# Performance work log

Measured on AMD Instinct MI355X. Metric: run time of the kernel, lower is better.

The kernel has to match this reference:

```python
import jax, jax.numpy as jnp
import numpy as np

B, DIM, H, W = 8, 96, 256, 256
NH, WS, SS = 3, 8, 4
HD = DIM // NH
SCALE = HD ** -0.5
N = WS * WS  # tokens per window


def _rel_pos_log(ws):
    # [N, N, 2] signed log relative coordinates (matches get_relative_positions)
    coords = np.stack(np.meshgrid(np.arange(ws), np.arange(ws), indexing='ij'))
    cf = coords.reshape(2, -1)
    rel = (cf[:, :, None] - cf[:, None, :]).transpose(1, 2, 0).astype(np.float32)
    return np.sign(rel) * np.log1p(np.abs(rel))


def _attn_mask(Hh, Ww, ws, ss):
    # Swin shifted-window mask: [nW, N, N] with 0 / -100
    img = np.zeros((Hh, Ww))
    cnt = 0
    sl = (slice(0, -ws), slice(-ws, -ss), slice(-ss, None))
    for h in sl:
        for w in sl:
            img[h, w] = cnt
            cnt += 1
    mw = img.reshape(Hh // ws, ws, Ww // ws, ws).transpose(0, 2, 1, 3).reshape(-1, ws * ws)
    am = mw[:, None, :] - mw[:, :, None]
    return np.where(am != 0, -100.0, 0.0).astype(np.float32)


REL_POS = jnp.asarray(_rel_pos_log(WS))        # [N, N, 2]
ATTN_MASK = jnp.asarray(_attn_mask(H, W, WS, SS))  # [nW, N, N]


def setup_inputs() -> dict:
    key = jax.random.key(0)
    ks = jax.random.split(key, 8)
    s = 0.02
    return {
        'x': jax.random.normal(ks[0], (B, DIM, H, W), jnp.float32),
        'V_w': jax.random.normal(ks[1], (DIM, DIM), jnp.float32) * s,
        'V_b': jnp.zeros((DIM,), jnp.float32),
        'QK_w': jax.random.normal(ks[2], (2 * DIM, DIM), jnp.float32) * s,
        'QK_b': jnp.zeros((2 * DIM,), jnp.float32),
        'proj_w': jax.random.normal(ks[3], (DIM, DIM), jnp.float32) * s,
        'proj_b': jnp.zeros((DIM,), jnp.float32),
        'dw_w': jax.random.normal(ks[4], (DIM, 5, 5), jnp.float32) * s,
        'dw_b': jnp.zeros((DIM,), jnp.float32),
        'meta_w1': jax.random.normal(ks[5], (256, 2), jnp.float32) * 0.1,
        'meta_b1': jnp.zeros((256,), jnp.float32),
        'meta_w2': jax.random.normal(ks[6], (NH, 256), jnp.float32) * 0.1,
        'meta_b2': jnp.zeros((NH,), jnp.float32),
    }


def reference(x, V_w, V_b, QK_w, QK_b, proj_w, proj_b, dw_w, dw_b,
              meta_w1, meta_b1, meta_w2, meta_b2):
    # 1x1 convs as channel matmuls
    V = jnp.einsum('bchw,oc->bohw', x, V_w) + V_b[None, :, None, None]
    QK = jnp.einsum('bchw,oc->bohw', x, QK_w) + QK_b[None, :, None, None]
    qkv = jnp.concatenate([QK, V], axis=1).transpose(0, 2, 3, 1)  # [B,H,W,3C]
    # cyclic shift
    qkv = jnp.roll(qkv, (-SS, -SS), axis=(1, 2))
    # window partition -> [B*nW, N, 3C]
    xw = qkv.reshape(B, H // WS, WS, W // WS, WS, 3 * DIM)
    xw = xw.transpose(0, 1, 3, 2, 4, 5).reshape(-1, N, 3 * DIM)
    qkv3 = xw.reshape(-1, N, 3, NH, HD).transpose(2, 0, 3, 1, 4)  # [3, B_, nh, N, hd]
    q, k, v = qkv3[0] * SCALE, qkv3[1], qkv3[2]
    attn = jnp.einsum('whnd,whmd->whnm', q, k)  # [B_, nh, N, N]
    # MLP relative-position bias
    bias = jax.nn.relu(REL_POS @ meta_w1.T + meta_b1) @ meta_w2.T + meta_b2  # [N,N,nh]
    attn = attn + bias.transpose(2, 0, 1)[None]
    nW = ATTN_MASK.shape[0]
    attn = attn.reshape(B, nW, NH, N, N) + ATTN_MASK[None, :, None]
    attn = jax.nn.softmax(attn, axis=-1).reshape(-1, NH, N, N)
    xo = jnp.einsum('whnm,whmd->wnhd', attn, v).reshape(-1, N, DIM)
    # window reverse -> [B,H,W,C]
    xr = xo.reshape(B, H // WS, W // WS, WS, WS, DIM)
    xr = xr.transpose(0, 1, 3, 2, 4, 5).reshape(B, H, W, DIM)
    xr = jnp.roll(xr, (SS, SS), axis=(1, 2)).transpose(0, 3, 1, 2)  # [B,C,H,W]
    # depthwise 5x5 conv with reflect padding on V
    Vp = jnp.pad(V, ((0, 0), (0, 0), (2, 2), (2, 2)), mode='reflect')
    conv_out = jax.lax.conv_general_dilated(
        Vp, dw_w.reshape(DIM, 1, 5, 5), (1, 1), 'VALID',
        feature_group_count=DIM,
        dimension_numbers=('NCHW', 'OIHW', 'NCHW')) + dw_b[None, :, None, None]
    out = jnp.einsum('bchw,oc->bohw', conv_out + xr, proj_w) + proj_b[None, :, None, None]
    return out
```

## Files before the change

kernel.cpp:

```cpp
#include <hip/hip_runtime.h>
#include <hip/hip_bf16.h>

#define HW 65536
#define SCALE_Q 0.17677669529663687f

typedef __bf16 bf16x8 __attribute__((ext_vector_type(8)));
typedef float f32x4 __attribute__((ext_vector_type(4)));

__global__ void bias_kernel(const float* __restrict__ w1, const float* __restrict__ b1,
                            const float* __restrict__ w2, const float* __restrict__ b2,
                            float* __restrict__ biasF) {
    int gid = blockIdx.x * blockDim.x + threadIdx.x;
    if (gid >= 12288) return;
    int lane = gid & 63, r = (gid >> 6) & 3, ni = (gid >> 8) & 3, mi = (gid >> 10) & 3, h = gid >> 12;
    int i = mi * 16 + ((lane >> 4) << 2) + r;
    int j = ni * 16 + (lane & 15);
    float di = (float)((i >> 3) - (j >> 3));
    float dj = (float)((i & 7) - (j & 7));
    float r0 = (di > 0.f ? 1.f : (di < 0.f ? -1.f : 0.f)) * log1pf(fabsf(di));
    float r1 = (dj > 0.f ? 1.f : (dj < 0.f ? -1.f : 0.f)) * log1pf(fabsf(dj));
    float acc = 0.f;
    for (int t = 0; t < 256; ++t) {
        float u = fmaf(w1[2 * t], r0, fmaf(w1[2 * t + 1], r1, b1[t]));
        u = fmaxf(u, 0.f);
        acc = fmaf(w2[h * 256 + t], u, acc);
    }
    biasF[gid] = acc + b2[h];
}

__global__ void wtrans_kernel(const float* __restrict__ QK_w, const float* __restrict__ V_w,
                              const float* __restrict__ proj_w,
                              __bf16* __restrict__ Whi, __bf16* __restrict__ Wlo,
                              __bf16* __restrict__ WpHi, __bf16* __restrict__ WpLo) {
    int idx = blockIdx.x * blockDim.x + threadIdx.x;
    if (idx < 288 * 96) {
        int oo = idx / 96, c = idx - oo * 96;
        int h = oo / 96, rem = oo - h * 96, grp = rem >> 5, d = rem & 31;
        float w = (grp == 0) ? QK_w[(h * 32 + d) * 96 + c]
                : (grp == 1) ? QK_w[(96 + h * 32 + d) * 96 + c]
                             : V_w[(h * 32 + d) * 96 + c];
        __bf16 hi = (__bf16)w;
        Whi[idx] = hi;
        Wlo[idx] = (__bf16)(w - (float)hi);
    } else if (idx < 288 * 96 + 96 * 96) {
        int rdx = idx - 288 * 96;
        float w = proj_w[rdx];
        __bf16 hi = (__bf16)w;
        WpHi[rdx] = hi;
        WpLo[rdx] = (__bf16)(w - (float)hi);
    }
}

template <bool XRB>
__global__ __launch_bounds__(256, 3) void fused_qkv_attn(
    const float* __restrict__ x,
    const __bf16* __restrict__ Whi, const __bf16* __restrict__ Wlo,
    const float* __restrict__ QK_b, const float* __restrict__ V_b,
    const float* __restrict__ biasF,
    unsigned short* __restrict__ Vout, void* __restrict__ xrv) {
    __shared__ __align__(16) char lds[53376];
    int tid = threadIdx.x;
    int w4 = tid >> 6;
    int lane = tid & 63;
    int l16 = lane & 15;
    int g8 = (lane >> 4) << 3;
    int g4 = (lane >> 4) << 2;
    int bx0 = blockIdx.x;
    int bxs = (bx0 & 7) * 256 + (bx0 >> 3);
    int b = bxs >> 8;
    int wh = (bxs >> 3) & 31;
    int ww0 = (bxs & 7) << 2;
    int wh8 = wh << 3;
    int wb8 = ww0 << 3;
    int ww = ww0 + w4;
    int ti = lane >> 3, tj = lane & 7;
    int ph = (wh8 + ti + 4) & 255;
    int pw = ((ww << 3) + tj + 4) & 255;
    int pos   = ph * 256 + pw;
    int pos_s = (wh8 + ti) * 256 + (ww << 3) + tj;

    __bf16* Xh = (__bf16*)lds;
    const float* xb = x + (size_t)b * 96 * HW;
    for (int idx = tid; idx < 24576; idx += 256) {
        int c = idx >> 8, r = (idx >> 5) & 7, col = idx & 31;
        int pph = (wh8 + r + 4) & 255;
        int ppw = (wb8 + col + 4) & 255;
        Xh[(col >> 3) * 6672 + (r * 8 + (col & 7)) * 104 + c] =
            (__bf16)xb[(size_t)c * HW + pph * 256 + ppw];
    }
    __syncthreads();

    bf16x8 Ah[4][3];
    const __bf16* Xw = Xh + w4 * 6672;
#pragma unroll
    for (int mi = 0; mi < 4; ++mi)
#pragma unroll
        for (int ks = 0; ks < 3; ++ks)
            Ah[mi][ks] = *(const bf16x8*)(Xw + (mi * 16 + l16) * 104 + ks * 32 + g8);
    __syncthreads();

    char* hb = lds + w4 * 9984;
    __bf16* slab = (__bf16*)hb;
    __bf16* Vt   = (__bf16*)(hb + 5120);
    float*  Xr   = (float*)hb;

    bool bhh = (wh == 31), bww = (ww == 31);
    int rc[4];
#pragma unroll
    for (int ni = 0; ni < 4; ++ni) {
        int t = ni * 16 + l16;
        rc[ni] = (bhh ? (((t >> 3) < 4) ? 1 : 2) : 0) * 3 + (bww ? (((t & 7) < 4) ? 1 : 2) : 0);
    }

#pragma unroll 1
    for (int h = 0; h < 3; ++h) {
        bf16x8 Qf[4], Kf[4];
        {
            f32x4 acc[4][2];
#pragma unroll
            for (int mi = 0; mi < 4; ++mi)
#pragma unroll
                for (int ni = 0; ni < 2; ++ni) acc[mi][ni] = (f32x4){0.f, 0.f, 0.f, 0.f};
            __builtin_amdgcn_s_setprio(1);
#pragma unroll
            for (int ks = 0; ks < 3; ++ks)
#pragma unroll
                for (int ni = 0; ni < 2; ++ni) {
                    bf16x8 Bh = *(const bf16x8*)(Whi + (h * 96 + ni * 16 + l16) * 96 + ks * 32 + g8);
#pragma unroll
                    for (int mi = 0; mi < 4; ++mi)
                        acc[mi][ni] = __builtin_amdgcn_mfma_f32_16x16x32_bf16(Ah[mi][ks], Bh, acc[mi][ni], 0, 0, 0);
                }
            __builtin_amdgcn_s_setprio(0);
#pragma unroll
            for (int ni = 0; ni < 2; ++ni) {
                float bias = QK_b[h * 32 + ni * 16 + l16];
#pragma unroll
                for (int mi = 0; mi < 4; ++mi)
#pragma unroll
                    for (int r = 0; r < 4; ++r)
                        slab[(mi * 16 + g4 + r) * 40 + ni * 16 + l16] = (__bf16)((acc[mi][ni][r] + bias) * SCALE_Q);
            }
#pragma unroll
            for (int mi = 0; mi < 4; ++mi) Qf[mi] = *(const bf16x8*)(slab + (mi * 16 + l16) * 40 + g8);
        }
        {
            f32x4 acc[4][2];
#pragma unroll
            for (int mi = 0; mi < 4; ++mi)
#pragma unroll
                for (int ni = 0; ni < 2; ++ni) acc[mi][ni] = (f32x4){0.f, 0.f, 0.f, 0.f};
            __builtin_amdgcn_s_setprio(1);
#pragma unroll
            for (int ks = 0; ks < 3; ++ks)
#pragma unroll
                for (int ni = 0; ni < 2; ++ni) {
                    bf16x8 Bh = *(const bf16x8*)(Whi + (h * 96 + 32 + ni * 16 + l16) * 96 + ks * 32 + g8);
#pragma unroll
                    for (int mi = 0; mi < 4; ++mi)
                        acc[mi][ni] = __builtin_amdgcn_mfma_f32_16x16x32_bf16(Ah[mi][ks], Bh, acc[mi][ni], 0, 0, 0);
                }
            __builtin_amdgcn_s_setprio(0);
#pragma unroll
            for (int ni = 0; ni < 2; ++ni) {
                float bias = QK_b[96 + h * 32 + ni * 16 + l16];
#pragma unroll
                for (int mi = 0; mi < 4; ++mi)
#pragma unroll
                    for (int r = 0; r < 4; ++r)
                        slab[(mi * 16 + g4 + r) * 40 + ni * 16 + l16] = (__bf16)(acc[mi][ni][r] + bias);
            }
#pragma unroll
            for (int mi = 0; mi < 4; ++mi) Kf[mi] = *(const bf16x8*)(slab + (mi * 16 + l16) * 40 + g8);
        }
        {
            f32x4 acc[4][2];
#pragma unroll
            for (int mi = 0; mi < 4; ++mi)
#pragma unroll
                for (int ni = 0; ni < 2; ++ni) acc[mi][ni] = (f32x4){0.f, 0.f, 0.f, 0.f};
            __builtin_amdgcn_s_setprio(1);
#pragma unroll
            for (int ks = 0; ks < 3; ++ks)
#pragma unroll
                for (int ni = 0; ni < 2; ++ni) {
                    int oo = (h * 96 + 64 + ni * 16 + l16) * 96 + ks * 32 + g8;
                    bf16x8 Bh = *(const bf16x8*)(Whi + oo);
                    bf16x8 Bl = *(const bf16x8*)(Wlo + oo);
#pragma unroll
                    for (int mi = 0; mi < 4; ++mi) {
                        acc[mi][ni] = __builtin_amdgcn_mfma_f32_16x16x32_bf16(Ah[mi][ks], Bh, acc[mi][ni], 0, 0, 0);
                        acc[mi][ni] = __builtin_amdgcn_mfma_f32_16x16x32_bf16(Ah[mi][ks], Bl, acc[mi][ni], 0, 0, 0);
                    }
                }
            __builtin_amdgcn_s_setprio(0);
#pragma unroll
            for (int ni = 0; ni < 2; ++ni) {
                float bias = V_b[h * 32 + ni * 16 + l16];
#pragma unroll
                for (int mi = 0; mi < 4; ++mi)
#pragma unroll
                    for (int r = 0; r < 4; ++r)
                        Vt[(ni * 16 + l16) * 72 + mi * 16 + g4 + r] = (__bf16)(acc[mi][ni][r] + bias);
            }
        }
#pragma unroll
        for (int d = 0; d < 32; ++d)
            Vout[(size_t)(b * 96 + h * 32 + d) * HW + pos_s] = ((const unsigned short*)Vt)[d * 72 + lane];

        f32x4 sc[4][4];
        __builtin_amdgcn_s_setprio(1);
#pragma unroll
        for (int mi = 0; mi < 4; ++mi)
#pragma unroll
            for (int ni = 0; ni < 4; ++ni) {
                sc[mi][ni] = (f32x4){0.f, 0.f, 0.f, 0.f};
                sc[mi][ni] = __builtin_amdgcn_mfma_f32_16x16x32_bf16(Qf[mi], Kf[ni], sc[mi][ni], 0, 0, 0);
            }
        __builtin_amdgcn_s_setprio(0);
        const float* bF = biasF + h * 4096;
#pragma unroll
        for (int mi = 0; mi < 4; ++mi)
#pragma unroll
            for (int r = 0; r < 4; ++r) {
                int row = mi * 16 + g4 + r;
                float s0 = sc[mi][0][r] + bF[((mi * 4 + 0) * 4 + r) * 64 + lane];
                float s1 = sc[mi][1][r] + bF[((mi * 4 + 1) * 4 + r) * 64 + lane];
                float s2 = sc[mi][2][r] + bF[((mi * 4 + 2) * 4 + r) * 64 + lane];
                float s3 = sc[mi][3][r] + bF[((mi * 4 + 3) * 4 + r) * 64 + lane];
                if (bhh || bww) {
                    int rr = (bhh ? (((row >> 3) < 4) ? 1 : 2) : 0) * 3 +
                             (bww ? (((row & 7) < 4) ? 1 : 2) : 0);
                    if (rr != rc[0]) s0 -= 100.f;
                    if (rr != rc[1]) s1 -= 100.f;
                    if (rr != rc[2]) s2 -= 100.f;
                    if (rr != rc[3]) s3 -= 100.f;
                }
                float mm = fmaxf(fmaxf(s0, s1), fmaxf(s2, s3));
                mm = fmaxf(mm, __shfl_xor(mm, 1));
                mm = fmaxf(mm, __shfl_xor(mm, 2));
                mm = fmaxf(mm, __shfl_xor(mm, 4));
                mm = fmaxf(mm, __shfl_xor(mm, 8));
                float e0 = __expf(s0 - mm), e1 = __expf(s1 - mm);
                float e2 = __expf(s2 - mm), e3 = __expf(s3 - mm);
                float sum = e0 + e1 + e2 + e3;
                sum += __shfl_xor(sum, 1);
                sum += __shfl_xor(sum, 2);
                sum += __shfl_xor(sum, 4);
                sum += __shfl_xor(sum, 8);
                float inv = 1.f / sum;
                sc[mi][0][r] = e0 * inv;
                sc[mi][1][r] = e1 * inv;
                sc[mi][2][r] = e2 * inv;
                sc[mi][3][r] = e3 * inv;
            }
        f32x4 po[4][2];
#pragma unroll
        for (int mi = 0; mi < 4; ++mi)
#pragma unroll
            for (int ni = 0; ni < 2; ++ni) po[mi][ni] = (f32x4){0.f, 0.f, 0.f, 0.f};
#pragma unroll
        for (int ks = 0; ks < 2; ++ks) {
#pragma unroll
            for (int mi = 0; mi < 4; ++mi)
#pragma unroll
                for (int r = 0; r < 4; ++r) {
                    int row = mi * 16 + g4 + r;
                    slab[row * 40 + l16]      = (__bf16)sc[mi][ks * 2 + 0][r];
                    slab[row * 40 + 16 + l16] = (__bf16)sc[mi][ks * 2 + 1][r];
                }
            bf16x8 Vf[2], Pf;
#pragma unroll
            for (int ni = 0; ni < 2; ++ni)
                Vf[ni] = *(const bf16x8*)(Vt + (ni * 16 + l16) * 72 + ks * 32 + g8);
            __builtin_amdgcn_s_setprio(1);
#pragma unroll
            for (int mi = 0; mi < 4; ++mi) {
                Pf = *(const bf16x8*)(slab + (mi * 16 + l16) * 40 + g8);
#pragma unroll
                for (int ni = 0; ni < 2; ++ni)
                    po[mi][ni] = __builtin_amdgcn_mfma_f32_16x16x32_bf16(Pf, Vf[ni], po[mi][ni], 0, 0, 0);
            }
            __builtin_amdgcn_s_setprio(0);
        }
#pragma unroll
        for (int mi = 0; mi < 4; ++mi)
#pragma unroll
            for (int ni = 0; ni < 2; ++ni)
#pragma unroll
                for (int r = 0; r < 4; ++r)
                    Xr[(mi * 16 + g4 + r) * 36 + ni * 16 + l16] = po[mi][ni][r];
        if constexpr (XRB) {
            unsigned short* xrg = (unsigned short*)xrv + (size_t)(b * 96 + h * 32) * HW + pos;
#pragma unroll
            for (int c4 = 0; c4 < 8; ++c4) {
                f32x4 v = *(const f32x4*)(Xr + lane * 36 + c4 * 4);
#pragma unroll
                for (int j = 0; j < 4; ++j) {
                    __bf16 t = (__bf16)v[j];
                    xrg[(size_t)(c4 * 4 + j) * HW] = *(unsigned short*)&t;
                }
            }
        } else {
            float* xrg = (float*)xrv + (size_t)(b * 96 + h * 32) * HW + pos;
#pragma unroll
            for (int c4 = 0; c4 < 8; ++c4) {
                f32x4 v = *(const f32x4*)(Xr + lane * 36 + c4 * 4);
                xrg[(size_t)(c4 * 4 + 0) * HW] = v[0];
                xrg[(size_t)(c4 * 4 + 1) * HW] = v[1];
                xrg[(size_t)(c4 * 4 + 2) * HW] = v[2];
                xrg[(size_t)(c4 * 4 + 3) * HW] = v[3];
            }
        }
    }
}

template <bool XRB>
__global__ __launch_bounds__(256) void dwproj_kernel(
    const __hip_bfloat16* __restrict__ Vs, const float* __restrict__ dw_w,
    const float* __restrict__ dw_b, const __bf16* __restrict__ WpHi,
    const __bf16* __restrict__ WpLo, const float* __restrict__ pb,
    const void* __restrict__ xrv, float* __restrict__ T) {
    __shared__ __align__(16) __bf16 Ts[13312];
    int bx0 = blockIdx.x;
    int bx = (bx0 & 7) * 512 + (bx0 >> 3);
    int half = bx & 1, h = (bx >> 1) & 255, b = bx >> 9;
    int w0 = half << 7;
    int tid = threadIdx.x;
    for (int task = tid; task < 1536; task += 256) {
        int c = task >> 4, g = task & 15;
        int wbase = w0 + (g << 3);
        const __hip_bfloat16* Vp = Vs + (size_t)(b * 96 + c) * HW;
        const float* wt = dw_w + c * 25;
        float acc[8];
        float bias = dw_b[c];
#pragma unroll
        for (int i = 0; i < 8; ++i) acc[i] = bias;
        bool fast = (wbase >= 8) && (wbase <= 240);
#pragma unroll
        for (int dy = -2; dy <= 2; ++dy) {
            int hh = h + dy;
            hh = hh < 0 ? -hh : (hh > 255 ? 510 - hh : hh);
            int hs = (hh + 252) & 255;
            const __hip_bfloat16* row = Vp + hs * 256;
            float xv[12];
            if (fast) {
                const uint* rp = (const uint*)(row + (wbase - 6));
#pragma unroll
                for (int g2 = 0; g2 < 6; ++g2) {
                    uint u = rp[g2];
                    xv[2 * g2]     = __uint_as_float(u << 16);
                    xv[2 * g2 + 1] = __uint_as_float(u & 0xffff0000u);
                }
            } else {
#pragma unroll
                for (int idx = 0; idx < 12; ++idx) {
                    int cw = wbase - 2 + idx;
                    cw = cw < 0 ? -cw : (cw > 255 ? 510 - cw : cw);
                    int cs = (cw + 252) & 255;
                    uint u = *(const unsigned short*)(row + cs);
                    xv[idx] = __uint_as_float(u << 16);
                }
            }
            const float* w5 = wt + (dy + 2) * 5;
#pragma unroll
            for (int dx = 0; dx < 5; ++dx) {
                float wv = w5[dx];
#pragma unroll
                for (int i = 0; i < 8; ++i) acc[i] = fmaf(wv, xv[i + dx], acc[i]);
            }
        }
        if constexpr (XRB) {
            const unsigned short* xp = (const unsigned short*)xrv + (size_t)(b * 96 + c) * HW + h * 256 + wbase;
            uint4 u = *(const uint4*)xp;
            acc[0] += __uint_as_float(u.x << 16);
            acc[1] += __uint_as_float(u.x & 0xffff0000u);
            acc[2] += __uint_as_float(u.y << 16);
            acc[3] += __uint_as_float(u.y & 0xffff0000u);
            acc[4] += __uint_as_float(u.z << 16);
            acc[5] += __uint_as_float(u.z & 0xffff0000u);
            acc[6] += __uint_as_float(u.w << 16);
            acc[7] += __uint_as_float(u.w & 0xffff0000u);
        } else {
            const float* xp = (const float*)xrv + (size_t)(b * 96 + c) * HW + h * 256;
            f32x4 x0 = *(const f32x4*)(xp + wbase);
            f32x4 x1 = *(const f32x4*)(xp + wbase + 4);
#pragma unroll
            for (int i = 0; i < 4; ++i) { acc[i] += x0[i]; acc[4 + i] += x1[i]; }
        }
#pragma unroll
        for (int i = 0; i < 8; ++i) Ts[(g * 8 + i) * 104 + c] = (__bf16)acc[i];
    }
    __syncthreads();
    int lane = tid & 63;
    int l16 = lane & 15;
    int g8 = (lane >> 4) << 3;
    int g4 = (lane >> 4) << 2;
    int wv = tid >> 6;
    f32x4 po[2][6];
#pragma unroll
    for (int mi = 0; mi < 2; ++mi)
#pragma unroll
        for (int ni = 0; ni < 6; ++ni) po[mi][ni] = (f32x4){0.f, 0.f, 0.f, 0.f};
#pragma unroll
    for (int ks = 0; ks < 3; ++ks) {
        bf16x8 Av[2];
#pragma unroll
        for (int mi = 0; mi < 2; ++mi)
            Av[mi] = *(const bf16x8*)(Ts + (wv * 32 + mi * 16 + l16) * 104 + ks * 32 + g8);
#pragma unroll
        for (int ni = 0; ni < 6; ++ni) {
            int o = ni * 16 + l16;
            bf16x8 Bh = *(const bf16x8*)(WpHi + o * 96 + ks * 32 + g8);
            bf16x8 Bl = *(const bf16x8*)(WpLo + o * 96 + ks * 32 + g8);
#pragma unroll
            for (int mi = 0; mi < 2; ++mi) {
                po[mi][ni] = __builtin_amdgcn_mfma_f32_16x16x32_bf16(Av[mi], Bh, po[mi][ni], 0, 0, 0);
                po[mi][ni] = __builtin_amdgcn_mfma_f32_16x16x32_bf16(Av[mi], Bl, po[mi][ni], 0, 0, 0);
            }
        }
    }
#pragma unroll
    for (int ni = 0; ni < 6; ++ni) {
        int o = ni * 16 + l16;
        float bias = pb[o];
#pragma unroll
        for (int mi = 0; mi < 2; ++mi) {
            f32x4 v = po[mi][ni];
            v[0] += bias; v[1] += bias; v[2] += bias; v[3] += bias;
            *(f32x4*)(T + (size_t)(b * 96 + o) * HW + h * 256 + w0 + wv * 32 + mi * 16 + g4) = v;
        }
    }
}

extern "C" void kernel_launch(void* const* d_in, const int* in_sizes, int n_in,
                              void* d_out, int out_size, void* d_ws, size_t ws_size,
                              hipStream_t stream) {
    const float* x      = (const float*)d_in[0];
    const float* V_w    = (const float*)d_in[1];
    const float* V_b    = (const float*)d_in[2];
    const float* QK_w   = (const float*)d_in[3];
    const float* QK_b   = (const float*)d_in[4];
    const float* proj_w = (const float*)d_in[5];
    const float* proj_b = (const float*)d_in[6];
    const float* dw_w   = (const float*)d_in[7];
    const float* dw_b   = (const float*)d_in[8];
    const float* mw1    = (const float*)d_in[9];
    const float* mb1    = (const float*)d_in[10];
    const float* mw2    = (const float*)d_in[11];
    const float* mb2    = (const float*)d_in[12];
    float* out = (float*)d_out;

    char* ws = (char*)d_ws;
    const size_t VB = 100663296;
    bool xrb = (ws_size >= 2 * VB + 49152 + 2 * 55296 + 2 * 18432);

    __hip_bfloat16* Vbuf = (__hip_bfloat16*)ws;
    size_t off = VB;
    unsigned short* xr16 = nullptr;
    if (xrb) { xr16 = (unsigned short*)(ws + off); off += VB; }
    float*  biasF = (float*)(ws + off); off += 49152;
    __bf16* Whi   = (__bf16*)(ws + off); off += 55296;
    __bf16* Wlo   = (__bf16*)(ws + off); off += 55296;
    __bf16* WpHi  = (__bf16*)(ws + off); off += 18432;
    __bf16* WpLo  = (__bf16*)(ws + off);

    bias_kernel<<<48, 256, 0, stream>>>(mw1, mb1, mw2, mb2, biasF);
    wtrans_kernel<<<144, 256, 0, stream>>>(QK_w, V_w, proj_w, Whi, Wlo, WpHi, WpLo);
    if (xrb) {
        fused_qkv_attn<true><<<2048, 256, 0, stream>>>(x, Whi, Wlo, QK_b, V_b, biasF,
                                                       (unsigned short*)Vbuf, (void*)xr16);
        dwproj_kernel<true><<<4096, 256, 0, stream>>>(Vbuf, dw_w, dw_b, WpHi, WpLo, proj_b,
                                                      (const void*)xr16, out);
    } else {
        fused_qkv_attn<false><<<2048, 256, 0, stream>>>(x, Whi, Wlo, QK_b, V_b, biasF,
                                                        (unsigned short*)Vbuf, (void*)out);
        dwproj_kernel<false><<<4096, 256, 0, stream>>>(Vbuf, dw_w, dw_b, WpHi, WpLo, proj_b,
                                                       (const void*)out, out);
    }
}
```

Baseline: 683.5 us.

## Coalesce V and attention-output stores via block-wide LDS staging; widen dwproj blocks

The attention kernel used to write V and the attention output one 2-byte element per lane per channel, scattered across 32 strided channel planes. It now stages both in LDS as bf16 and, after a block barrier, writes each row of 32 contiguous pixels with 16-byte vector stores. The roll shift moves to the consumer, which reads two 8-byte halves at shifted columns. The dwproj kernel goes to 512 threads, each wave handling 16 rows instead of 32, to raise parallelism. The change adds two barriers per head, and the fallback fp32 path now rounds the attention output through bf16.

```diff
diff --git a/kernel.cpp b/kernel.cpp
--- a/kernel.cpp
+++ b/kernel.cpp
@@ -73,11 +73,6 @@
     int wh8 = wh << 3;
     int wb8 = ww0 << 3;
     int ww = ww0 + w4;
-    int ti = lane >> 3, tj = lane & 7;
-    int ph = (wh8 + ti + 4) & 255;
-    int pw = ((ww << 3) + tj + 4) & 255;
-    int pos   = ph * 256 + pw;
-    int pos_s = (wh8 + ti) * 256 + (ww << 3) + tj;
 
     __bf16* Xh = (__bf16*)lds;
     const float* xb = x + (size_t)b * 96 * HW;
@@ -102,7 +97,6 @@
     char* hb = lds + w4 * 9984;
     __bf16* slab = (__bf16*)hb;
     __bf16* Vt   = (__bf16*)(hb + 5120);
-    float*  Xr   = (float*)hb;
 
     bool bhh = (wh == 31), bww = (ww == 31);
     int rc[4];
@@ -111,6 +105,7 @@
         int t = ni * 16 + l16;
         rc[ni] = (bhh ? (((t >> 3) < 4) ? 1 : 2) : 0) * 3 + (bww ? (((t & 7) < 4) ? 1 : 2) : 0);
     }
+    int dd = tid >> 3, tt = tid & 7;
 
 #pragma unroll 1
     for (int h = 0; h < 3; ++h) {
@@ -204,9 +199,6 @@
                         Vt[(ni * 16 + l16) * 72 + mi * 16 + g4 + r] = (__bf16)(acc[mi][ni][r] + bias);
             }
         }
-#pragma unroll
-        for (int d = 0; d < 32; ++d)
-            Vout[(size_t)(b * 96 + h * 32 + d) * HW + pos_s] = ((const unsigned short*)Vt)[d * 72 + lane];
 
         f32x4 sc[4][4];
         __builtin_amdgcn_s_setprio(1);
@@ -283,40 +275,49 @@
             }
             __builtin_amdgcn_s_setprio(0);
         }
+        __bf16* Xrt = slab;
 #pragma unroll
         for (int mi = 0; mi < 4; ++mi)
 #pragma unroll
             for (int ni = 0; ni < 2; ++ni)
 #pragma unroll
                 for (int r = 0; r < 4; ++r)
-                    Xr[(mi * 16 + g4 + r) * 36 + ni * 16 + l16] = po[mi][ni][r];
-        if constexpr (XRB) {
-            unsigned short* xrg = (unsigned short*)xrv + (size_t)(b * 96 + h * 32) * HW + pos;
-#pragma unroll
-            for (int c4 = 0; c4 < 8; ++c4) {
-                f32x4 v = *(const f32x4*)(Xr + lane * 36 + c4 * 4);
-#pragma unroll
-                for (int j = 0; j < 4; ++j) {
-                    __bf16 t = (__bf16)v[j];
-                    xrg[(size_t)(c4 * 4 + j) * HW] = *(unsigned short*)&t;
-                }
-            }
-        } else {
-            float* xrg = (float*)xrv + (size_t)(b * 96 + h * 32) * HW + pos;
-#pragma unroll
-            for (int c4 = 0; c4 < 8; ++c4) {
-                f32x4 v = *(const f32x4*)(Xr + lane * 36 + c4 * 4);
-                xrg[(size_t)(c4 * 4 + 0) * HW] = v[0];
-                xrg[(size_t)(c4 * 4 + 1) * HW] = v[1];
-                xrg[(size_t)(c4 * 4 + 2) * HW] = v[2];
-                xrg[(size_t)(c4 * 4 + 3) * HW] = v[3];
-            }
-        }
+                    Xrt[(ni * 16 + l16) * 72 + mi * 16 + g4 + r] = (__bf16)po[mi][ni][r];
+        __syncthreads();
+
+        {
+            unsigned short* dstV = Vout + (size_t)(b * 96 + h * 32 + dd) * HW + (wh8 + tt) * 256 + wb8;
+#pragma unroll
+            for (int w = 0; w < 4; ++w) {
+                uint4 v = *(const uint4*)(lds + w * 9984 + 5120 + dd * 144 + tt * 16);
+                *(uint4*)(dstV + w * 8) = v;
+            }
+            if constexpr (XRB) {
+                unsigned short* dstX = (unsigned short*)xrv + (size_t)(b * 96 + h * 32 + dd) * HW +
+                                       ((wh8 + tt + 4) & 255) * 256 + wb8;
+#pragma unroll
+                for (int w = 0; w < 4; ++w) {
+                    uint4 v = *(const uint4*)(lds + w * 9984 + dd * 144 + tt * 16);
+                    *(uint4*)(dstX + w * 8) = v;
+                }
+            } else {
+                float* dstX = (float*)xrv + (size_t)(b * 96 + h * 32 + dd) * HW +
+                              ((wh8 + tt + 4) & 255) * 256;
+#pragma unroll
+                for (int w = 0; w < 4; ++w) {
+                    const __bf16* s = (const __bf16*)(lds + w * 9984 + dd * 144 + tt * 16);
+#pragma unroll
+                    for (int j = 0; j < 8; ++j)
+                        dstX[(wb8 + 4 + w * 8 + j) & 255] = (float)s[j];
+                }
+            }
+        }
+        __syncthreads();
     }
 }
 
 template <bool XRB>
-__global__ __launch_bounds__(256) void dwproj_kernel(
+__global__ __launch_bounds__(512) void dwproj_kernel(
     const __hip_bfloat16* __restrict__ Vs, const float* __restrict__ dw_w,
     const float* __restrict__ dw_b, const __bf16* __restrict__ WpHi,
     const __bf16* __restrict__ WpLo, const float* __restrict__ pb,
@@ -327,7 +328,7 @@
     int half = bx & 1, h = (bx >> 1) & 255, b = bx >> 9;
     int w0 = half << 7;
     int tid = threadIdx.x;
-    for (int task = tid; task < 1536; task += 256) {
+    for (int task = tid; task < 1536; task += 512) {
         int c = task >> 4, g = task & 15;
         int wbase = w0 + (g << 3);
         const __hip_bfloat16* Vp = Vs + (size_t)(b * 96 + c) * HW;
@@ -371,16 +372,18 @@
             }
         }
         if constexpr (XRB) {
-            const unsigned short* xp = (const unsigned short*)xrv + (size_t)(b * 96 + c) * HW + h * 256 + wbase;
-            uint4 u = *(const uint4*)xp;
-            acc[0] += __uint_as_float(u.x << 16);
-            acc[1] += __uint_as_float(u.x & 0xffff0000u);
-            acc[2] += __uint_as_float(u.y << 16);
-            acc[3] += __uint_as_float(u.y & 0xffff0000u);
-            acc[4] += __uint_as_float(u.z << 16);
-            acc[5] += __uint_as_float(u.z & 0xffff0000u);
-            acc[6] += __uint_as_float(u.w << 16);
-            acc[7] += __uint_as_float(u.w & 0xffff0000u);
+            const unsigned short* xrow = (const unsigned short*)xrv + (size_t)(b * 96 + c) * HW + h * 256;
+            int c0 = (wbase + 252) & 255;
+            uint2 A = *(const uint2*)(xrow + c0);
+            uint2 B = *(const uint2*)(xrow + wbase);
+            acc[0] += __uint_as_float(A.x << 16);
+            acc[1] += __uint_as_float(A.x & 0xffff0000u);
+            acc[2] += __uint_as_float(A.y << 16);
+            acc[3] += __uint_as_float(A.y & 0xffff0000u);
+            acc[4] += __uint_as_float(B.x << 16);
+            acc[5] += __uint_as_float(B.x & 0xffff0000u);
+            acc[6] += __uint_as_float(B.y << 16);
+            acc[7] += __uint_as_float(B.y & 0xffff0000u);
         } else {
             const float* xp = (const float*)xrv + (size_t)(b * 96 + c) * HW + h * 256;
             f32x4 x0 = *(const f32x4*)(xp + wbase);
@@ -397,39 +400,28 @@
     int g8 = (lane >> 4) << 3;
     int g4 = (lane >> 4) << 2;
     int wv = tid >> 6;
-    f32x4 po[2][6];
-#pragma unroll
-    for (int mi = 0; mi < 2; ++mi)
-#pragma unroll
-        for (int ni = 0; ni < 6; ++ni) po[mi][ni] = (f32x4){0.f, 0.f, 0.f, 0.f};
+    f32x4 po[6];
+#pragma unroll
+    for (int ni = 0; ni < 6; ++ni) po[ni] = (f32x4){0.f, 0.f, 0.f, 0.f};
 #pragma unroll
     for (int ks = 0; ks < 3; ++ks) {
-        bf16x8 Av[2];
-#pragma unroll
-        for (int mi = 0; mi < 2; ++mi)
-            Av[mi] = *(const bf16x8*)(Ts + (wv * 32 + mi * 16 + l16) * 104 + ks * 32 + g8);
+        bf16x8 Av = *(const bf16x8*)(Ts + (wv * 16 + l16) * 104 + ks * 32 + g8);
 #pragma unroll
         for (int ni = 0; ni < 6; ++ni) {
             int o = ni * 16 + l16;
             bf16x8 Bh = *(const bf16x8*)(WpHi + o * 96 + ks * 32 + g8);
             bf16x8 Bl = *(const bf16x8*)(WpLo + o * 96 + ks * 32 + g8);
-#pragma unroll
-            for (int mi = 0; mi < 2; ++mi) {
-                po[mi][ni] = __builtin_amdgcn_mfma_f32_16x16x32_bf16(Av[mi], Bh, po[mi][ni], 0, 0, 0);
-                po[mi][ni] = __builtin_amdgcn_mfma_f32_16x16x32_bf16(Av[mi], Bl, po[mi][ni], 0, 0, 0);
-            }
+            po[ni] = __builtin_amdgcn_mfma_f32_16x16x32_bf16(Av, Bh, po[ni], 0, 0, 0);
+            po[ni] = __builtin_amdgcn_mfma_f32_16x16x32_bf16(Av, Bl, po[ni], 0, 0, 0);
         }
     }
 #pragma unroll
     for (int ni = 0; ni < 6; ++ni) {
         int o = ni * 16 + l16;
         float bias = pb[o];
-#pragma unroll
-        for (int mi = 0; mi < 2; ++mi) {
-            f32x4 v = po[mi][ni];
-            v[0] += bias; v[1] += bias; v[2] += bias; v[3] += bias;
-            *(f32x4*)(T + (size_t)(b * 96 + o) * HW + h * 256 + w0 + wv * 32 + mi * 16 + g4) = v;
-        }
+        f32x4 v = po[ni];
+        v[0] += bias; v[1] += bias; v[2] += bias; v[3] += bias;
+        *(f32x4*)(T + (size_t)(b * 96 + o) * HW + h * 256 + w0 + wv * 16 + g4) = v;
     }
 }
 
@@ -470,12 +462,12 @@
     if (xrb) {
         fused_qkv_attn<true><<<2048, 256, 0, stream>>>(x, Whi, Wlo, QK_b, V_b, biasF,
                                                        (unsigned short*)Vbuf, (void*)xr16);
-        dwproj_kernel<true><<<4096, 256, 0, stream>>>(Vbuf, dw_w, dw_b, WpHi, WpLo, proj_b,
+        dwproj_kernel<true><<<4096, 512, 0, stream>>>(Vbuf, dw_w, dw_b, WpHi, WpLo, proj_b,
                                                       (const void*)xr16, out);
     } else {
         fused_qkv_attn<false><<<2048, 256, 0, stream>>>(x, Whi, Wlo, QK_b, V_b, biasF,
                                                         (unsigned short*)Vbuf, (void*)out);
-        dwproj_kernel<false><<<4096, 256, 0, stream>>>(Vbuf, dw_w, dw_b, WpHi, WpLo, proj_b,
+        dwproj_kernel<false><<<4096, 512, 0, stream>>>(Vbuf, dw_w, dw_b, WpHi, WpLo, proj_b,
                                                        (const void*)out, out);
     }
 }
```

Result: slower. 717.0 us (+4.9%).
